# Kernel optimization log

Hardware: AMD Instinct MI355X
Metric: run time of the kernel (lower is better)

Reference implementation:

```python
import jax, jax.numpy as jnp
import numpy as np

B, T, D, H = 2, 2048, 1024, 16
Dh = D // H
MAX_LEN = 2048


def build_rope_cache(max_len, head_dim):
    theta = 10000.0 ** (-jnp.arange(0, head_dim, 2, dtype=jnp.float32) / head_dim)
    pos = jnp.arange(max_len, dtype=jnp.float32)
    angles = pos[:, None] * theta[None, :]          # [T, Dh/2]
    sin = jnp.sin(angles)[:, None, :]               # [T, 1, Dh/2]
    cos = jnp.cos(angles)[:, None, :]
    return sin, cos


def apply_rotary_pos_emb(q, k, sin, cos):
    q1, q2 = jnp.split(q, 2, axis=-1)
    k1, k2 = jnp.split(k, 2, axis=-1)
    q_out = jnp.concatenate([q1 * cos + q2 * sin, -q1 * sin + q2 * cos], axis=-1)
    k_out = jnp.concatenate([k1 * cos + k2 * sin, -k1 * sin + k2 * cos], axis=-1)
    return q_out, k_out


def setup_inputs() -> dict:
    key = jax.random.key(0)
    k1, k2, k3 = jax.random.split(key, 3)
    x = jax.random.normal(k1, (B, T, D), dtype=jnp.float32)
    W_qkv = jax.random.normal(k2, (D, 3 * D), dtype=jnp.float32) * (D ** -0.5)
    W_proj = jax.random.normal(k3, (D, D), dtype=jnp.float32) * (D ** -0.5)
    # causal mask: 1.0 where attention is disallowed (future positions)
    mask = jnp.triu(jnp.ones((T, T), dtype=jnp.float32), k=1)
    return {"x": x, "mask": mask, "W_qkv": W_qkv, "W_proj": W_proj}


def reference(x, mask, W_qkv, W_proj):
    b, t, d = x.shape
    qkv = x @ W_qkv                                  # [B,T,3D]
    q, k, v = jnp.split(qkv, 3, axis=-1)
    q = q.reshape(b, t, H, Dh)
    k = k.reshape(b, t, H, Dh)
    v = v.reshape(b, t, H, Dh)
    sin, cos = build_rope_cache(MAX_LEN, Dh)
    q, k = apply_rotary_pos_emb(q, k, sin[:t], cos[:t])
    scale = 1.0 / jnp.sqrt(jnp.float32(Dh))
    att = jnp.einsum('bthd,bThd->bhtT', q, k) * scale
    att = att + mask * -1e9                          # mask broadcasts [T,T]->[B,H,T,T]
    weights = jax.nn.softmax(att, axis=-1)
    out = jnp.einsum('bhtT,bThd->bthd', weights, v).reshape(b, t, d)
    return out @ W_proj
```

## Files before the change

kernel.cpp:

```cpp
#include <hip/hip_runtime.h>
#include <hip/hip_bf16.h>

typedef __bf16  bf16x8 __attribute__((ext_vector_type(8)));
typedef __bf16  bf16x4 __attribute__((ext_vector_type(4)));
typedef __bf16  bf16x2 __attribute__((ext_vector_type(2)));
typedef float   f32x4  __attribute__((ext_vector_type(4)));
typedef float   f32x16 __attribute__((ext_vector_type(16)));
typedef unsigned u32x4 __attribute__((ext_vector_type(4)));

#define MFMA16(a,b,c) __builtin_amdgcn_mfma_f32_16x16x32_bf16(a,b,c,0,0,0)
#define MFMA32(a,b,c) __builtin_amdgcn_mfma_f32_32x32x16_bf16(a,b,c,0,0,0)


struct bf4 { __hip_bfloat16 a,b,c,d; };

__global__ __launch_bounds__(256) void cast_f32_bf16(const float* __restrict__ in,
                                                     __hip_bfloat16* __restrict__ out,
                                                     int n4) {
  int i = blockIdx.x * 256 + threadIdx.x;
  if (i >= n4) return;
  float4 v = ((const float4*)in)[i];
  bf4 o { __float2bfloat16(v.x), __float2bfloat16(v.y),
          __float2bfloat16(v.z), __float2bfloat16(v.w) };
  ((bf4*)out)[i] = o;
}

__global__ __launch_bounds__(256) void transpose_cast(const float* __restrict__ W,
                                                      __hip_bfloat16* __restrict__ WT,
                                                      int R, int C) {
  __shared__ float tile[32][33];
  int c0 = blockIdx.x * 32, r0 = blockIdx.y * 32;
  int tx = threadIdx.x & 31, ty = threadIdx.x >> 5;
  #pragma unroll
  for (int i = 0; i < 32; i += 8)
    tile[ty + i][tx] = W[(size_t)(r0 + ty + i) * C + c0 + tx];
  __syncthreads();
  #pragma unroll
  for (int i = 0; i < 32; i += 8)
    WT[(size_t)(c0 + ty + i) * R + r0 + tx] = __float2bfloat16(tile[tx][ty + i]);
}

template <typename OutT>
__global__ __launch_bounds__(256) void gemm_bt(const __hip_bfloat16* __restrict__ A,
                                               const __hip_bfloat16* __restrict__ BT,
                                               OutT* __restrict__ C,
                                               int M, int N, int K) {
  __shared__ __hip_bfloat16 As[2][128][32];
  __shared__ __hip_bfloat16 Bs[2][128][32];
  int tid  = threadIdx.x;
  int lane = tid & 63, wid = tid >> 6;
  int wm = wid >> 1, wn = wid & 1;
  int rowBase = blockIdx.y * 128;
  int colBase = blockIdx.x * 128;
  int lr = lane & 15, lg = lane >> 4;

  f32x4 acc[4][4];
  #pragma unroll
  for (int i = 0; i < 4; ++i)
    #pragma unroll
    for (int j = 0; j < 4; ++j) acc[i][j] = f32x4{0.f,0.f,0.f,0.f};

  int nt = K >> 5;

#define GSTAGE(buf, kt)                                                                 \
  do {                                                                                  \
    int k0_ = (kt) << 5;                                                                \
    _Pragma("unroll")                                                                   \
    for (int p = 0; p < 2; ++p) {                                                       \
      int idx = p * 256 + tid;                                                          \
      int r_ = idx >> 2, sl_ = idx & 3;                                                 \
      __builtin_amdgcn_global_load_lds(                                                 \
        (const __attribute__((address_space(1))) unsigned int*)                         \
          &A[(size_t)(rowBase + r_) * K + k0_ + ((sl_ ^ (r_ & 3)) * 8)],                \
        (__attribute__((address_space(3))) unsigned int*)&As[buf][r_][sl_ * 8], 16, 0, 0);\
      __builtin_amdgcn_global_load_lds(                                                 \
        (const __attribute__((address_space(1))) unsigned int*)                         \
          &BT[(size_t)(colBase + r_) * K + k0_ + ((sl_ ^ (r_ & 3)) * 8)],               \
        (__attribute__((address_space(3))) unsigned int*)&Bs[buf][r_][sl_ * 8], 16, 0, 0);\
    }                                                                                   \
  } while (0)

  GSTAGE(0, 0);
  for (int t = 0; t < nt; ++t) {
    int cur = t & 1;
    if (t + 1 < nt) {
      GSTAGE(cur ^ 1, t + 1);
      asm volatile("s_waitcnt vmcnt(4)" ::: "memory");
    } else {
      asm volatile("s_waitcnt vmcnt(0)" ::: "memory");
    }
    __builtin_amdgcn_s_barrier();
    __builtin_amdgcn_sched_barrier(0);

    bf16x8 af[4], bfr[4];
    #pragma unroll
    for (int mf = 0; mf < 4; ++mf) {
      int row = wm*64 + mf*16 + lr;
      af[mf]  = *(const bf16x8*)&As[cur][row][((lg ^ (lr & 3)) * 8)];
    }
    #pragma unroll
    for (int nf = 0; nf < 4; ++nf) {
      int row = wn*64 + nf*16 + lr;
      bfr[nf] = *(const bf16x8*)&Bs[cur][row][((lg ^ (lr & 3)) * 8)];
    }
    #pragma unroll
    for (int mf = 0; mf < 4; ++mf)
      #pragma unroll
      for (int nf = 0; nf < 4; ++nf)
        acc[mf][nf] = MFMA16(af[mf], bfr[nf], acc[mf][nf]);

    __builtin_amdgcn_s_barrier();
  }
#undef GSTAGE

  #pragma unroll
  for (int mf = 0; mf < 4; ++mf)
    #pragma unroll
    for (int nf = 0; nf < 4; ++nf)
      #pragma unroll
      for (int r = 0; r < 4; ++r) {
        int row = rowBase + wm*64 + mf*16 + lg*4 + r;
        int col = colBase + wn*64 + nf*16 + lr;
        float v = acc[mf][nf][r];
        if constexpr (sizeof(OutT) == 2) C[(size_t)row * N + col] = __float2bfloat16(v);
        else                             C[(size_t)row * N + col] = v;
      }
}

__global__ __launch_bounds__(256) void build_sincos(float2* __restrict__ tbl) {
  int idx = blockIdx.x * 256 + threadIdx.x;
  int i = idx & 31, t = idx >> 5;
  float theta = expf(-9.210340371976184f * (float)i * 0.03125f);
  float sn, cs;
  sincosf((float)t * theta, &sn, &cs);
  tbl[idx] = float2{sn, cs};
}

__global__ __launch_bounds__(256) void rope_qk(const __hip_bfloat16* __restrict__ qkv,
                                               const float2* __restrict__ tbl,
                                               __hip_bfloat16* __restrict__ Qb,
                                               __hip_bfloat16* __restrict__ Kb) {
  int idx = blockIdx.x * 256 + threadIdx.x;
  int i8 = idx & 3;
  int h  = (idx >> 2) & 15;
  int t  = (idx >> 6) & 2047;
  int b  = idx >> 17;
  int i0 = i8 * 8;
  size_t row = (size_t)(b * 2048 + t) * 3072;
  bf16x8 q1 = *(const bf16x8*)&qkv[row + h*64 + i0];
  bf16x8 q2 = *(const bf16x8*)&qkv[row + h*64 + 32 + i0];
  bf16x8 k1 = *(const bf16x8*)&qkv[row + 1024 + h*64 + i0];
  bf16x8 k2 = *(const bf16x8*)&qkv[row + 1024 + h*64 + 32 + i0];
  const float2* tb = &tbl[(t << 5) + i0];

  const float QS = 0.18033688011112042f;
  bf16x8 qo1, qo2, ko1, ko2;
  #pragma unroll
  for (int e = 0; e < 8; ++e) {
    float2 sc = tb[e];
    float sn = sc.x, cs = sc.y;
    float a = (float)q1[e], bb = (float)q2[e];
    float c = (float)k1[e], dd = (float)k2[e];
    qo1[e] = (__bf16)(( a*cs + bb*sn) * QS);
    qo2[e] = (__bf16)((-a*sn + bb*cs) * QS);
    ko1[e] = (__bf16)( c*cs + dd*sn);
    ko2[e] = (__bf16)(-c*sn + dd*cs);
  }
  size_t qkbase = ((size_t)(b*16 + h) * 2048 + t) * 64;
  *(bf16x8*)&Qb[qkbase + i0]      = qo1;
  *(bf16x8*)&Qb[qkbase + 32 + i0] = qo2;
  *(bf16x8*)&Kb[qkbase + i0]      = ko1;
  *(bf16x8*)&Kb[qkbase + 32 + i0] = ko2;
}

__global__ __launch_bounds__(256) void v_transpose(const __hip_bfloat16* __restrict__ qkv,
                                                   __hip_bfloat16* __restrict__ Vt) {
  __shared__ __hip_bfloat16 tile[64][66];
  int blk = blockIdx.x;
  int tb = blk & 31, hh = (blk >> 5) & 15, bb = blk >> 9;
  int t0 = tb * 64;
  int tid = threadIdx.x;
  int row = tid >> 2, dc = (tid & 3) * 16;
  const __hip_bfloat16* src = qkv + (size_t)(bb*2048 + t0 + row) * 3072 + 2048 + hh*64 + dc;
  *(bf16x8*)&tile[row][dc]     = *(const bf16x8*)&src[0];
  *(bf16x8*)&tile[row][dc + 8] = *(const bf16x8*)&src[8];
  __syncthreads();
  int d = tid >> 2, tc = (tid & 3) * 16;
  __hip_bfloat16 outv[16];
  #pragma unroll
  for (int k = 0; k < 16; ++k) outv[k] = tile[tc + k][d];
  __hip_bfloat16* dst = Vt + ((size_t)(bb*16 + hh) * 64 + d) * 2048 + t0 + tc;
  *(bf16x8*)&dst[0] = *(bf16x8*)&outv[0];
  *(bf16x8*)&dst[8] = *(bf16x8*)&outv[8];
}

__device__ __forceinline__ unsigned pk2(float lo, float hi_) {
  bf16x2 t; t[0] = (__bf16)lo; t[1] = (__bf16)hi_;
  return __builtin_bit_cast(unsigned, t);
}

__global__ __launch_bounds__(512) void attn_chunk(const __hip_bfloat16* __restrict__ Qb,
                                                  const __hip_bfloat16* __restrict__ Kb,
                                                  const __hip_bfloat16* __restrict__ Vt,
                                                  __hip_bfloat16* __restrict__ Opart,
                                                  float* __restrict__ sbuf) {
  __shared__ __hip_bfloat16 Ks[2][2048];
  __shared__ __hip_bfloat16 Vs[2][2048];
  int tid = threadIdx.x;
  int wid = tid >> 6, lane = tid & 63;
  int ql = lane & 31, hi = lane >> 5;

  int bid = blockIdx.x;
  int bh, c, jbase, lenmax; bool diag;
  if (bid < 384) {
    bh = bid / 12; int pr = bid % 12;
    if (pr < 6)       { c = 0; jbase = 16 + 8*pr; }
    else if (pr < 10) { c = 1; jbase = 32 + 8*(pr-6); }
    else              { c = 2; jbase = 48 + 8*(pr-10); }
    lenmax = 16; diag = false;
  } else {
    int e = bid - 384;
    int hh = (e < 128) ? 1 : 0;
    int e2 = e & 127;
    bh = e2 >> 2; c = e2 & 3;
    jbase = 16*c + 8*hh; lenmax = 8*hh + 8; diag = true;
  }
  int j = jbase + wid;
  int len = diag ? ((j & 15) + 1) : 16;
  int q0 = j * 32, t0 = c * 512;
  int jobid;
  if (!diag) jobid = (c == 0) ? (j - 16) : ((c == 1) ? (j + 16) : (j + 32));
  else       jobid = 96 + ((15 - (j & 15)) << 2) + c;
  int job = jobid * 32 + bh;

  const __hip_bfloat16* Qp = Qb + (size_t)bh * 2048 * 64;
  const __hip_bfloat16* Kp = Kb + (size_t)bh * 2048 * 64;
  const __hip_bfloat16* Vp = Vt + (size_t)bh * 64 * 2048;

  bf16x8 qf[4];
  #pragma unroll
  for (int cc = 0; cc < 4; ++cc)
    qf[cc] = *(const bf16x8*)&Qp[(size_t)(q0 + ql) * 64 + cc*16 + hi*8];

  f32x16 o0, o1;
  #pragma unroll
  for (int r = 0; r < 16; ++r) { o0[r] = 0.f; o1[r] = 0.f; }
  float s = 0.f;

  int kr = tid >> 3, ksl = tid & 7;
  int vjj = tid - 256;
  int ve  = (vjj >> 4) & 1;
  int vx  = vjj ^ (ve << 2);
  int vr  = vx >> 2;
  int vtc = (vx & 3) ^ (vr & 3);

#define ASTAGE(buf, it_)                                                                \
  do {                                                                                  \
    int kv0_ = t0 + (it_) * 32;                                                         \
    if (tid < 256)                                                                      \
      __builtin_amdgcn_global_load_lds(                                                 \
        (const __attribute__((address_space(1))) unsigned int*)                         \
          &Kp[(size_t)(kv0_ + kr) * 64 + ((ksl ^ (kr & 7)) * 8)],                       \
        (__attribute__((address_space(3))) unsigned int*)&Ks[buf][tid * 8], 16, 0, 0);  \
    else                                                                                \
      __builtin_amdgcn_global_load_lds(                                                 \
        (const __attribute__((address_space(1))) unsigned int*)                         \
          &Vp[(size_t)vr * 2048 + kv0_ + vtc * 8],                                      \
        (__attribute__((address_space(3))) unsigned int*)&Vs[buf][vjj * 8], 16, 0, 0);  \
  } while (0)

  ASTAGE(0, 0);
  for (int it = 0; it < lenmax; ++it) {
    int cur = it & 1;
    if (it + 1 < lenmax) {
      ASTAGE(cur ^ 1, it + 1);
      asm volatile("s_waitcnt vmcnt(1)" ::: "memory");
    } else {
      asm volatile("s_waitcnt vmcnt(0)" ::: "memory");
    }
    __builtin_amdgcn_s_barrier();
    __builtin_amdgcn_sched_barrier(0);

    if (it < len) {
      int kv0 = t0 + it * 32;
      bf16x8 kf[4], vf[4];
      #pragma unroll
      for (int cc = 0; cc < 4; ++cc)
        kf[cc] = *(const bf16x8*)&Ks[cur][ql * 64 + (((cc*2 + hi) ^ (ql & 7)) * 8)];
      #pragma unroll
      for (int g = 0; g < 2; ++g)
        #pragma unroll
        for (int cc = 0; cc < 2; ++cc) {
          int d_ = g*32 + ql, tc_ = cc*2 + hi;
          int L = (d_*4 + (tc_ ^ (d_ & 3))) ^ (((d_ >> 2) & 1) << 2);
          vf[g*2 + cc] = *(const bf16x8*)&Vs[cur][L * 8];
        }

      f32x16 st;
      #pragma unroll
      for (int r = 0; r < 16; ++r) st[r] = 0.f;
      #pragma unroll
      for (int cc = 0; cc < 4; ++cc) st = MFMA32(kf[cc], qf[cc], st);

      if (diag && it == len - 1) {
        #pragma unroll
        for (int r = 0; r < 16; ++r) {
          int kv = kv0 + (r & 3) + 8*(r >> 2) + 4*hi;
          if (kv > q0 + ql) st[r] = -1e30f;
        }
      }

      float p[16]; float ps = 0.f;
      #pragma unroll
      for (int r = 0; r < 16; ++r) { p[r] = exp2f(st[r]); ps += p[r]; }
      ps += __shfl_xor(ps, 32);
      s += ps;

      bf16x8 pb[2];
      #pragma unroll
      for (int cc = 0; cc < 2; ++cc) {
        unsigned w0 = pk2(p[cc*8+0], p[cc*8+1]);
        unsigned w1 = pk2(p[cc*8+2], p[cc*8+3]);
        unsigned w2 = pk2(p[cc*8+4], p[cc*8+5]);
        unsigned w3 = pk2(p[cc*8+6], p[cc*8+7]);
        unsigned r0 = __shfl_xor(hi ? w0 : w2, 32);
        unsigned r1 = __shfl_xor(hi ? w1 : w3, 32);
        u32x4 pw;
        pw[0] = hi ? r0 : w0;
        pw[1] = hi ? r1 : w1;
        pw[2] = hi ? w2 : r0;
        pw[3] = hi ? w3 : r1;
        pb[cc] = __builtin_bit_cast(bf16x8, pw);
      }

      o0 = MFMA32(vf[0], pb[0], o0);
      o0 = MFMA32(vf[1], pb[1], o0);
      o1 = MFMA32(vf[2], pb[0], o1);
      o1 = MFMA32(vf[3], pb[1], o1);
    }
    __builtin_amdgcn_s_barrier();
  }
#undef ASTAGE

  __hip_bfloat16* Op = Opart + (size_t)job * 2048 + ql * 64;
  #pragma unroll
  for (int rr = 0; rr < 4; ++rr) {
    bf16x4 w;
    #pragma unroll
    for (int e = 0; e < 4; ++e) w[e] = (__bf16)o0[rr*4 + e];
    *(bf16x4*)&Op[8*rr + 4*hi] = w;
  }
  #pragma unroll
  for (int rr = 0; rr < 4; ++rr) {
    bf16x4 w;
    #pragma unroll
    for (int e = 0; e < 4; ++e) w[e] = (__bf16)o1[rr*4 + e];
    *(bf16x4*)&Op[32 + 8*rr + 4*hi] = w;
  }
  if (hi == 0) sbuf[(size_t)job * 32 + ql] = s;
}

__global__ __launch_bounds__(64) void attn_combine(const __hip_bfloat16* __restrict__ Opart,
                                                   const float* __restrict__ sbuf,
                                                   __hip_bfloat16* __restrict__ Ob) {
  int bid2 = blockIdx.x;
  int j = bid2 >> 5, bh = bid2 & 31;
  int h = bh & 15, b = bh >> 4;
  int tid = threadIdx.x, ql = tid & 31, half = tid >> 5;
  int nc = (j >> 4) + 1;

  int gs[4];
  const int Sseg[3] = {0, 48, 80};
  #pragma unroll
  for (int i = 0; i < 3; ++i)
    if (i < nc - 1) gs[i] = (Sseg[i] + j - 16*(i+1)) * 32 + bh;
  gs[nc-1] = (96 + 4*(15 - (j & 15)) + (j >> 4)) * 32 + bh;

  float Ssum = 0.f;
  #pragma unroll
  for (int i = 0; i < 4; ++i)
    if (i < nc) Ssum += sbuf[(size_t)gs[i]*32 + ql];

  float acc[32];
  #pragma unroll
  for (int e = 0; e < 32; ++e) acc[e] = 0.f;
  #pragma unroll
  for (int i = 0; i < 4; ++i)
    if (i < nc) {
      const bf16x8* src = (const bf16x8*)(Opart + (size_t)gs[i]*2048 + ql*64 + half*32);
      #pragma unroll
      for (int q4 = 0; q4 < 4; ++q4) {
        bf16x8 v = src[q4];
        #pragma unroll
        for (int e = 0; e < 8; ++e) acc[q4*8 + e] += (float)v[e];
      }
    }

  float inv = 1.f / Ssum;
  size_t row = (size_t)b * 2048 + j*32 + ql;
  __hip_bfloat16* dst = Ob + row * 1024 + h*64 + half*32;
  #pragma unroll
  for (int q4 = 0; q4 < 4; ++q4) {
    bf16x8 w;
    #pragma unroll
    for (int e = 0; e < 8; ++e) w[e] = (__bf16)(acc[q4*8 + e] * inv);
    *(bf16x8*)&dst[q4*8] = w;
  }
}

extern "C" void kernel_launch(void* const* d_in, const int* in_sizes, int n_in,
                              void* d_out, int out_size, void* d_ws, size_t ws_size,
                              hipStream_t stream) {
  const float* x     = (const float*)d_in[0];
  const float* Wqkv  = (const float*)d_in[2];
  const float* Wproj = (const float*)d_in[3];
  float* out = (float*)d_out;

  char* ws = (char*)d_ws;
  const size_t MB = 1024 * 1024;
  __hip_bfloat16* xb  = (__hip_bfloat16*)(ws);
  __hip_bfloat16* Wqt = (__hip_bfloat16*)(ws +  8*MB);
  __hip_bfloat16* Wpt = (__hip_bfloat16*)(ws + 14*MB);
  __hip_bfloat16* qkv = (__hip_bfloat16*)(ws + 16*MB);
  __hip_bfloat16* Qb  = (__hip_bfloat16*)(ws + 40*MB);
  __hip_bfloat16* Kb  = (__hip_bfloat16*)(ws + 48*MB);
  __hip_bfloat16* Vt  = (__hip_bfloat16*)(ws + 56*MB);
  __hip_bfloat16* Ob  = (__hip_bfloat16*)(ws + 64*MB);
  __hip_bfloat16* Opart = (__hip_bfloat16*)(ws + 16*MB);
  float*          sbuf  = (float*)(ws + 36*MB);
  float2*         sctbl = (float2*)(ws + 8*MB);

  cast_f32_bf16<<<4096, 256, 0, stream>>>(x, xb, 1048576);
  transpose_cast<<<dim3(96, 32), 256, 0, stream>>>(Wqkv, Wqt, 1024, 3072);
  transpose_cast<<<dim3(32, 32), 256, 0, stream>>>(Wproj, Wpt, 1024, 1024);
  gemm_bt<__hip_bfloat16><<<dim3(24, 32), 256, 0, stream>>>(xb, Wqt, qkv, 4096, 3072, 1024);
  build_sincos<<<256, 256, 0, stream>>>(sctbl);
  rope_qk<<<1024, 256, 0, stream>>>(qkv, sctbl, Qb, Kb);
  v_transpose<<<1024, 256, 0, stream>>>(qkv, Vt);
  attn_chunk<<<640, 512, 0, stream>>>(Qb, Kb, Vt, Opart, sbuf);
  attn_combine<<<2048, 64, 0, stream>>>(Opart, sbuf, Ob);
  gemm_bt<float><<<dim3(8, 32), 256, 0, stream>>>(Ob, Wpt, out, 4096, 1024, 1024);
}
```

Before: 131.0 us.

## Stage 64-key KV tiles per barrier in attention chunk kernel

Doubles the K/V tile staged into shared memory per pipeline step from 32 to 64 keys. Every thread now issues one K and one V async load, and the LDS swizzle for V changes to match. Each staged tile is consumed as two 32-key sub-steps. This halves the number of barriers and wait points per block, at the cost of double the LDS footprint, which may reduce occupancy, and some wasted staging on diagonal blocks with odd lengths.

```diff
diff --git a/kernel.cpp b/kernel.cpp
--- a/kernel.cpp
+++ b/kernel.cpp
@@ -204,8 +204,8 @@
                                                   const __hip_bfloat16* __restrict__ Vt,
                                                   __hip_bfloat16* __restrict__ Opart,
                                                   float* __restrict__ sbuf) {
-  __shared__ __hip_bfloat16 Ks[2][2048];
-  __shared__ __hip_bfloat16 Vs[2][2048];
+  __shared__ __hip_bfloat16 Ks[2][4096];
+  __shared__ __hip_bfloat16 Vs[2][4096];
   int tid = threadIdx.x;
   int wid = tid >> 6, lane = tid & 63;
   int ql = lane & 31, hi = lane >> 5;
@@ -226,8 +226,9 @@
     jbase = 16*c + 8*hh; lenmax = 8*hh + 8; diag = true;
   }
   int j = jbase + wid;
-  int len = diag ? ((j & 15) + 1) : 16;
+  int len32 = diag ? ((j & 15) + 1) : 16;
   int q0 = j * 32, t0 = c * 512;
+  int lenmax64 = lenmax >> 1;
   int jobid;
   if (!diag) jobid = (c == 0) ? (j - 16) : ((c == 1) ? (j + 16) : (j + 32));
   else       jobid = 96 + ((15 - (j & 15)) << 2) + c;
@@ -247,96 +248,96 @@
   for (int r = 0; r < 16; ++r) { o0[r] = 0.f; o1[r] = 0.f; }
   float s = 0.f;
 
-  int kr = tid >> 3, ksl = tid & 7;
-  int vjj = tid - 256;
-  int ve  = (vjj >> 4) & 1;
-  int vx  = vjj ^ (ve << 2);
-  int vr  = vx >> 2;
-  int vtc = (vx & 3) ^ (vr & 3);
+  int gr = tid >> 3, gsl = tid & 7;
+  int gsrc = gsl ^ (gr & 7);
 
 #define ASTAGE(buf, it_)                                                                \
   do {                                                                                  \
-    int kv0_ = t0 + (it_) * 32;                                                         \
-    if (tid < 256)                                                                      \
-      __builtin_amdgcn_global_load_lds(                                                 \
-        (const __attribute__((address_space(1))) unsigned int*)                         \
-          &Kp[(size_t)(kv0_ + kr) * 64 + ((ksl ^ (kr & 7)) * 8)],                       \
-        (__attribute__((address_space(3))) unsigned int*)&Ks[buf][tid * 8], 16, 0, 0);  \
-    else                                                                                \
-      __builtin_amdgcn_global_load_lds(                                                 \
-        (const __attribute__((address_space(1))) unsigned int*)                         \
-          &Vp[(size_t)vr * 2048 + kv0_ + vtc * 8],                                      \
-        (__attribute__((address_space(3))) unsigned int*)&Vs[buf][vjj * 8], 16, 0, 0);  \
+    int kvb_ = t0 + (it_) * 64;                                                         \
+    __builtin_amdgcn_global_load_lds(                                                   \
+      (const __attribute__((address_space(1))) unsigned int*)                           \
+        &Kp[(size_t)(kvb_ + gr) * 64 + gsrc * 8],                                       \
+      (__attribute__((address_space(3))) unsigned int*)&Ks[buf][tid * 8], 16, 0, 0);    \
+    __builtin_amdgcn_global_load_lds(                                                   \
+      (const __attribute__((address_space(1))) unsigned int*)                           \
+        &Vp[(size_t)gr * 2048 + kvb_ + gsrc * 8],                                       \
+      (__attribute__((address_space(3))) unsigned int*)&Vs[buf][tid * 8], 16, 0, 0);    \
   } while (0)
 
   ASTAGE(0, 0);
-  for (int it = 0; it < lenmax; ++it) {
+  for (int it = 0; it < lenmax64; ++it) {
     int cur = it & 1;
-    if (it + 1 < lenmax) {
+    if (it + 1 < lenmax64) {
       ASTAGE(cur ^ 1, it + 1);
-      asm volatile("s_waitcnt vmcnt(1)" ::: "memory");
+      asm volatile("s_waitcnt vmcnt(2)" ::: "memory");
     } else {
       asm volatile("s_waitcnt vmcnt(0)" ::: "memory");
     }
     __builtin_amdgcn_s_barrier();
     __builtin_amdgcn_sched_barrier(0);
 
-    if (it < len) {
-      int kv0 = t0 + it * 32;
-      bf16x8 kf[4], vf[4];
-      #pragma unroll
-      for (int cc = 0; cc < 4; ++cc)
-        kf[cc] = *(const bf16x8*)&Ks[cur][ql * 64 + (((cc*2 + hi) ^ (ql & 7)) * 8)];
-      #pragma unroll
-      for (int g = 0; g < 2; ++g)
+    #pragma unroll
+    for (int ss = 0; ss < 2; ++ss) {
+      int s32 = it * 2 + ss;
+      if (s32 < len32) {
+        int kv0 = t0 + s32 * 32;
+        bf16x8 kf[4], vf[4];
+        #pragma unroll
+        for (int cc = 0; cc < 4; ++cc) {
+          int krow = ss*32 + ql;
+          kf[cc] = *(const bf16x8*)&Ks[cur][(krow*8 + ((cc*2 + hi) ^ (krow & 7))) * 8];
+        }
+        #pragma unroll
+        for (int g = 0; g < 2; ++g)
+          #pragma unroll
+          for (int cc = 0; cc < 2; ++cc) {
+            int d_ = g*32 + ql;
+            int tc_ = ss*4 + cc*2 + hi;
+            vf[g*2 + cc] = *(const bf16x8*)&Vs[cur][(d_*8 + (tc_ ^ (d_ & 7))) * 8];
+          }
+
+        f32x16 st;
+        #pragma unroll
+        for (int r = 0; r < 16; ++r) st[r] = 0.f;
+        #pragma unroll
+        for (int cc = 0; cc < 4; ++cc) st = MFMA32(kf[cc], qf[cc], st);
+
+        if (diag && s32 == len32 - 1) {
+          #pragma unroll
+          for (int r = 0; r < 16; ++r) {
+            int kv = kv0 + (r & 3) + 8*(r >> 2) + 4*hi;
+            if (kv > q0 + ql) st[r] = -1e30f;
+          }
+        }
+
+        float p[16]; float ps = 0.f;
+        #pragma unroll
+        for (int r = 0; r < 16; ++r) { p[r] = exp2f(st[r]); ps += p[r]; }
+        ps += __shfl_xor(ps, 32);
+        s += ps;
+
+        bf16x8 pb[2];
         #pragma unroll
         for (int cc = 0; cc < 2; ++cc) {
-          int d_ = g*32 + ql, tc_ = cc*2 + hi;
-          int L = (d_*4 + (tc_ ^ (d_ & 3))) ^ (((d_ >> 2) & 1) << 2);
-          vf[g*2 + cc] = *(const bf16x8*)&Vs[cur][L * 8];
+          unsigned w0 = pk2(p[cc*8+0], p[cc*8+1]);
+          unsigned w1 = pk2(p[cc*8+2], p[cc*8+3]);
+          unsigned w2 = pk2(p[cc*8+4], p[cc*8+5]);
+          unsigned w3 = pk2(p[cc*8+6], p[cc*8+7]);
+          unsigned r0 = __shfl_xor(hi ? w0 : w2, 32);
+          unsigned r1 = __shfl_xor(hi ? w1 : w3, 32);
+          u32x4 pw;
+          pw[0] = hi ? r0 : w0;
+          pw[1] = hi ? r1 : w1;
+          pw[2] = hi ? w2 : r0;
+          pw[3] = hi ? w3 : r1;
+          pb[cc] = __builtin_bit_cast(bf16x8, pw);
         }
 
-      f32x16 st;
-      #pragma unroll
-      for (int r = 0; r < 16; ++r) st[r] = 0.f;
-      #pragma unroll
-      for (int cc = 0; cc < 4; ++cc) st = MFMA32(kf[cc], qf[cc], st);
-
-      if (diag && it == len - 1) {
-        #pragma unroll
-        for (int r = 0; r < 16; ++r) {
-          int kv = kv0 + (r & 3) + 8*(r >> 2) + 4*hi;
-          if (kv > q0 + ql) st[r] = -1e30f;
-        }
+        o0 = MFMA32(vf[0], pb[0], o0);
+        o0 = MFMA32(vf[1], pb[1], o0);
+        o1 = MFMA32(vf[2], pb[0], o1);
+        o1 = MFMA32(vf[3], pb[1], o1);
       }
-
-      float p[16]; float ps = 0.f;
-      #pragma unroll
-      for (int r = 0; r < 16; ++r) { p[r] = exp2f(st[r]); ps += p[r]; }
-      ps += __shfl_xor(ps, 32);
-      s += ps;
-
-      bf16x8 pb[2];
-      #pragma unroll
-      for (int cc = 0; cc < 2; ++cc) {
-        unsigned w0 = pk2(p[cc*8+0], p[cc*8+1]);
-        unsigned w1 = pk2(p[cc*8+2], p[cc*8+3]);
-        unsigned w2 = pk2(p[cc*8+4], p[cc*8+5]);
-        unsigned w3 = pk2(p[cc*8+6], p[cc*8+7]);
-        unsigned r0 = __shfl_xor(hi ? w0 : w2, 32);
-        unsigned r1 = __shfl_xor(hi ? w1 : w3, 32);
-        u32x4 pw;
-        pw[0] = hi ? r0 : w0;
-        pw[1] = hi ? r1 : w1;
-        pw[2] = hi ? w2 : r0;
-        pw[3] = hi ? w3 : r1;
-        pb[cc] = __builtin_bit_cast(bf16x8, pw);
-      }
-
-      o0 = MFMA32(vf[0], pb[0], o0);
-      o0 = MFMA32(vf[1], pb[1], o0);
-      o1 = MFMA32(vf[2], pb[0], o1);
-      o1 = MFMA32(vf[3], pb[1], o1);
     }
     __builtin_amdgcn_s_barrier();
   }
```

Result: slower. 142.9 us (+9.1%).

## Fuse RoPE and V transpose into QKV GEMM epilogue

Applied to the files above, without the earlier changes.

Adds a gemm_qkv kernel whose epilogue applies rotary embedding and the Q scale directly to the accumulators for Q/K column tiles, and transposes V tiles through shared memory into the Vt layout. This removes the bf16 qkv intermediate write and read and two separate kernel launches (rope_qk, v_transpose). The trade-offs are scalar 2-byte scattered stores in the Q/K epilogue and extra shared memory per block. The sincos table is moved to a different workspace offset.

```diff
diff --git a/kernel.cpp b/kernel.cpp
--- a/kernel.cpp
+++ b/kernel.cpp
@@ -40,13 +40,26 @@
     WT[(size_t)(c0 + ty + i) * R + r0 + tx] = __float2bfloat16(tile[tx][ty + i]);
 }
 
-template <typename OutT>
-__global__ __launch_bounds__(256) void gemm_bt(const __hip_bfloat16* __restrict__ A,
-                                               const __hip_bfloat16* __restrict__ BT,
-                                               OutT* __restrict__ C,
-                                               int M, int N, int K) {
-  __shared__ __hip_bfloat16 As[2][128][32];
-  __shared__ __hip_bfloat16 Bs[2][128][32];
+__global__ __launch_bounds__(256) void build_sincos(float2* __restrict__ tbl) {
+  int idx = blockIdx.x * 256 + threadIdx.x;
+  int i = idx & 31, t = idx >> 5;
+  float theta = expf(-9.210340371976184f * (float)i * 0.03125f);
+  float sn, cs;
+  sincosf((float)t * theta, &sn, &cs);
+  tbl[idx] = float2{sn, cs};
+}
+
+__global__ __launch_bounds__(256) void gemm_qkv(const __hip_bfloat16* __restrict__ A,
+                                                const __hip_bfloat16* __restrict__ BT,
+                                                const float2* __restrict__ tbl,
+                                                __hip_bfloat16* __restrict__ Qb,
+                                                __hip_bfloat16* __restrict__ Kb,
+                                                __hip_bfloat16* __restrict__ Vt) {
+  __shared__ __align__(16) char smem[34816];
+  auto As = (__hip_bfloat16 (*)[128][32])(smem);
+  auto Bs = (__hip_bfloat16 (*)[128][32])(smem + 16384);
+  auto Vl = (__hip_bfloat16 (*)[136])(smem);
+  const int K = 1024;
   int tid  = threadIdx.x;
   int lane = tid & 63, wid = tid >> 6;
   int wm = wid >> 1, wn = wid & 1;
@@ -113,6 +126,127 @@
   }
 #undef GSTAGE
 
+  int region = colBase >> 10;
+  int b = rowBase >> 11;
+  if (region < 2) {
+    const float QS = 0.18033688011112042f;
+    __hip_bfloat16* dst = (region == 0) ? Qb : Kb;
+    float scale = (region == 0) ? QS : 1.0f;
+    int h = ((colBase & 1023) >> 6) + wn;
+    #pragma unroll
+    for (int mf = 0; mf < 4; ++mf)
+      #pragma unroll
+      for (int r = 0; r < 4; ++r) {
+        int row = rowBase + wm*64 + mf*16 + lg*4 + r;
+        int t = row & 2047;
+        #pragma unroll
+        for (int nf = 0; nf < 2; ++nf) {
+          int i = nf*16 + lr;
+          float2 sc = tbl[(t << 5) + i];
+          float v1 = acc[mf][nf][r], v2 = acc[mf][nf+2][r];
+          size_t base = ((size_t)((b*16 + h) * 2048 + t)) * 64;
+          dst[base + i]      = __float2bfloat16(( v1*sc.y + v2*sc.x) * scale);
+          dst[base + 32 + i] = __float2bfloat16((-v1*sc.x + v2*sc.y) * scale);
+        }
+      }
+  } else {
+    #pragma unroll
+    for (int nf = 0; nf < 4; ++nf) {
+      int d = wn*64 + nf*16 + lr;
+      #pragma unroll
+      for (int mf = 0; mf < 4; ++mf) {
+        bf16x4 w;
+        #pragma unroll
+        for (int r = 0; r < 4; ++r) w[r] = (__bf16)acc[mf][nf][r];
+        *(bf16x4*)&Vl[d][wm*64 + mf*16 + lg*4] = w;
+      }
+    }
+    __syncthreads();
+    int vd = tid >> 1, half = tid & 1;
+    int h = ((colBase - 2048) >> 6) + (vd >> 6);
+    int dloc = vd & 63;
+    __hip_bfloat16* dstp = Vt + ((size_t)(b*16 + h) * 64 + dloc) * 2048
+                              + (rowBase & 2047) + half*64;
+    const __hip_bfloat16* srcp = &Vl[vd][half*64];
+    #pragma unroll
+    for (int g = 0; g < 8; ++g)
+      *(bf16x8*)&dstp[g*8] = *(const bf16x8*)&srcp[g*8];
+  }
+}
+
+template <typename OutT>
+__global__ __launch_bounds__(256) void gemm_bt(const __hip_bfloat16* __restrict__ A,
+                                               const __hip_bfloat16* __restrict__ BT,
+                                               OutT* __restrict__ C,
+                                               int M, int N, int K) {
+  __shared__ __hip_bfloat16 As[2][128][32];
+  __shared__ __hip_bfloat16 Bs[2][128][32];
+  int tid  = threadIdx.x;
+  int lane = tid & 63, wid = tid >> 6;
+  int wm = wid >> 1, wn = wid & 1;
+  int rowBase = blockIdx.y * 128;
+  int colBase = blockIdx.x * 128;
+  int lr = lane & 15, lg = lane >> 4;
+
+  f32x4 acc[4][4];
+  #pragma unroll
+  for (int i = 0; i < 4; ++i)
+    #pragma unroll
+    for (int j = 0; j < 4; ++j) acc[i][j] = f32x4{0.f,0.f,0.f,0.f};
+
+  int nt = K >> 5;
+
+#define GSTAGE(buf, kt)                                                                 \
+  do {                                                                                  \
+    int k0_ = (kt) << 5;                                                                \
+    _Pragma("unroll")                                                                   \
+    for (int p = 0; p < 2; ++p) {                                                       \
+      int idx = p * 256 + tid;                                                          \
+      int r_ = idx >> 2, sl_ = idx & 3;                                                 \
+      __builtin_amdgcn_global_load_lds(                                                 \
+        (const __attribute__((address_space(1))) unsigned int*)                         \
+          &A[(size_t)(rowBase + r_) * K + k0_ + ((sl_ ^ (r_ & 3)) * 8)],                \
+        (__attribute__((address_space(3))) unsigned int*)&As[buf][r_][sl_ * 8], 16, 0, 0);\
+      __builtin_amdgcn_global_load_lds(                                                 \
+        (const __attribute__((address_space(1))) unsigned int*)                         \
+          &BT[(size_t)(colBase + r_) * K + k0_ + ((sl_ ^ (r_ & 3)) * 8)],               \
+        (__attribute__((address_space(3))) unsigned int*)&Bs[buf][r_][sl_ * 8], 16, 0, 0);\
+    }                                                                                   \
+  } while (0)
+
+  GSTAGE(0, 0);
+  for (int t = 0; t < nt; ++t) {
+    int cur = t & 1;
+    if (t + 1 < nt) {
+      GSTAGE(cur ^ 1, t + 1);
+      asm volatile("s_waitcnt vmcnt(4)" ::: "memory");
+    } else {
+      asm volatile("s_waitcnt vmcnt(0)" ::: "memory");
+    }
+    __builtin_amdgcn_s_barrier();
+    __builtin_amdgcn_sched_barrier(0);
+
+    bf16x8 af[4], bfr[4];
+    #pragma unroll
+    for (int mf = 0; mf < 4; ++mf) {
+      int row = wm*64 + mf*16 + lr;
+      af[mf]  = *(const bf16x8*)&As[cur][row][((lg ^ (lr & 3)) * 8)];
+    }
+    #pragma unroll
+    for (int nf = 0; nf < 4; ++nf) {
+      int row = wn*64 + nf*16 + lr;
+      bfr[nf] = *(const bf16x8*)&Bs[cur][row][((lg ^ (lr & 3)) * 8)];
+    }
+    #pragma unroll
+    for (int mf = 0; mf < 4; ++mf)
+      #pragma unroll
+      for (int nf = 0; nf < 4; ++nf)
+        acc[mf][nf] = MFMA16(af[mf], bfr[nf], acc[mf][nf]);
+
+    __builtin_amdgcn_s_barrier();
+  }
+#undef GSTAGE
+
   #pragma unroll
   for (int mf = 0; mf < 4; ++mf)
     #pragma unroll
@@ -125,73 +259,6 @@
         if constexpr (sizeof(OutT) == 2) C[(size_t)row * N + col] = __float2bfloat16(v);
         else                             C[(size_t)row * N + col] = v;
       }
-}
-
-__global__ __launch_bounds__(256) void build_sincos(float2* __restrict__ tbl) {
-  int idx = blockIdx.x * 256 + threadIdx.x;
-  int i = idx & 31, t = idx >> 5;
-  float theta = expf(-9.210340371976184f * (float)i * 0.03125f);
-  float sn, cs;
-  sincosf((float)t * theta, &sn, &cs);
-  tbl[idx] = float2{sn, cs};
-}
-
-__global__ __launch_bounds__(256) void rope_qk(const __hip_bfloat16* __restrict__ qkv,
-                                               const float2* __restrict__ tbl,
-                                               __hip_bfloat16* __restrict__ Qb,
-                                               __hip_bfloat16* __restrict__ Kb) {
-  int idx = blockIdx.x * 256 + threadIdx.x;
-  int i8 = idx & 3;
-  int h  = (idx >> 2) & 15;
-  int t  = (idx >> 6) & 2047;
-  int b  = idx >> 17;
-  int i0 = i8 * 8;
-  size_t row = (size_t)(b * 2048 + t) * 3072;
-  bf16x8 q1 = *(const bf16x8*)&qkv[row + h*64 + i0];
-  bf16x8 q2 = *(const bf16x8*)&qkv[row + h*64 + 32 + i0];
-  bf16x8 k1 = *(const bf16x8*)&qkv[row + 1024 + h*64 + i0];
-  bf16x8 k2 = *(const bf16x8*)&qkv[row + 1024 + h*64 + 32 + i0];
-  const float2* tb = &tbl[(t << 5) + i0];
-
-  const float QS = 0.18033688011112042f;
-  bf16x8 qo1, qo2, ko1, ko2;
-  #pragma unroll
-  for (int e = 0; e < 8; ++e) {
-    float2 sc = tb[e];
-    float sn = sc.x, cs = sc.y;
-    float a = (float)q1[e], bb = (float)q2[e];
-    float c = (float)k1[e], dd = (float)k2[e];
-    qo1[e] = (__bf16)(( a*cs + bb*sn) * QS);
-    qo2[e] = (__bf16)((-a*sn + bb*cs) * QS);
-    ko1[e] = (__bf16)( c*cs + dd*sn);
-    ko2[e] = (__bf16)(-c*sn + dd*cs);
-  }
-  size_t qkbase = ((size_t)(b*16 + h) * 2048 + t) * 64;
-  *(bf16x8*)&Qb[qkbase + i0]      = qo1;
-  *(bf16x8*)&Qb[qkbase + 32 + i0] = qo2;
-  *(bf16x8*)&Kb[qkbase + i0]      = ko1;
-  *(bf16x8*)&Kb[qkbase + 32 + i0] = ko2;
-}
-
-__global__ __launch_bounds__(256) void v_transpose(const __hip_bfloat16* __restrict__ qkv,
-                                                   __hip_bfloat16* __restrict__ Vt) {
-  __shared__ __hip_bfloat16 tile[64][66];
-  int blk = blockIdx.x;
-  int tb = blk & 31, hh = (blk >> 5) & 15, bb = blk >> 9;
-  int t0 = tb * 64;
-  int tid = threadIdx.x;
-  int row = tid >> 2, dc = (tid & 3) * 16;
-  const __hip_bfloat16* src = qkv + (size_t)(bb*2048 + t0 + row) * 3072 + 2048 + hh*64 + dc;
-  *(bf16x8*)&tile[row][dc]     = *(const bf16x8*)&src[0];
-  *(bf16x8*)&tile[row][dc + 8] = *(const bf16x8*)&src[8];
-  __syncthreads();
-  int d = tid >> 2, tc = (tid & 3) * 16;
-  __hip_bfloat16 outv[16];
-  #pragma unroll
-  for (int k = 0; k < 16; ++k) outv[k] = tile[tc + k][d];
-  __hip_bfloat16* dst = Vt + ((size_t)(bb*16 + hh) * 64 + d) * 2048 + t0 + tc;
-  *(bf16x8*)&dst[0] = *(bf16x8*)&outv[0];
-  *(bf16x8*)&dst[8] = *(bf16x8*)&outv[8];
 }
 
 __device__ __forceinline__ unsigned pk2(float lo, float hi_) {
@@ -421,22 +488,19 @@
   __hip_bfloat16* xb  = (__hip_bfloat16*)(ws);
   __hip_bfloat16* Wqt = (__hip_bfloat16*)(ws +  8*MB);
   __hip_bfloat16* Wpt = (__hip_bfloat16*)(ws + 14*MB);
-  __hip_bfloat16* qkv = (__hip_bfloat16*)(ws + 16*MB);
   __hip_bfloat16* Qb  = (__hip_bfloat16*)(ws + 40*MB);
   __hip_bfloat16* Kb  = (__hip_bfloat16*)(ws + 48*MB);
   __hip_bfloat16* Vt  = (__hip_bfloat16*)(ws + 56*MB);
   __hip_bfloat16* Ob  = (__hip_bfloat16*)(ws + 64*MB);
   __hip_bfloat16* Opart = (__hip_bfloat16*)(ws + 16*MB);
   float*          sbuf  = (float*)(ws + 36*MB);
-  float2*         sctbl = (float2*)(ws + 8*MB);
+  float2*         sctbl = (float2*)(ws + 37*MB);
 
   cast_f32_bf16<<<4096, 256, 0, stream>>>(x, xb, 1048576);
   transpose_cast<<<dim3(96, 32), 256, 0, stream>>>(Wqkv, Wqt, 1024, 3072);
   transpose_cast<<<dim3(32, 32), 256, 0, stream>>>(Wproj, Wpt, 1024, 1024);
-  gemm_bt<__hip_bfloat16><<<dim3(24, 32), 256, 0, stream>>>(xb, Wqt, qkv, 4096, 3072, 1024);
   build_sincos<<<256, 256, 0, stream>>>(sctbl);
-  rope_qk<<<1024, 256, 0, stream>>>(qkv, sctbl, Qb, Kb);
-  v_transpose<<<1024, 256, 0, stream>>>(qkv, Vt);
+  gemm_qkv<<<dim3(24, 32), 256, 0, stream>>>(xb, Wqt, sctbl, Qb, Kb, Vt);
   attn_chunk<<<640, 512, 0, stream>>>(Qb, Kb, Vt, Opart, sbuf);
   attn_combine<<<2048, 64, 0, stream>>>(Opart, sbuf, Ob);
   gemm_bt<float><<<dim3(8, 32), 256, 0, stream>>>(Ob, Wpt, out, 4096, 1024, 1024);
```

Result: faster. 123.9 us (-5.4%).
